# Kernel tuning notes

Hardware: AMD Instinct MI355X
Metric: run time of the kernel (lower is better)

The kernel has to match this reference:

```python
import jax, jax.numpy as jnp
import numpy as np

N = 100000      # nodes
E = 3200000     # edges (avg degree 32)
D = 128         # input feature dim
K = 8           # propagation hops
OUT = 128       # output size


def setup_inputs() -> dict:
    key = jax.random.key(0)
    k1, k2, k3, k4 = jax.random.split(key, 4)
    feature = jax.random.normal(k1, (N, D), dtype=jnp.float32)
    edge_index = jax.random.randint(k2, (2, E), 0, N, dtype=jnp.int32)
    # nn.Linear default init: U(-1/sqrt(fan_in), 1/sqrt(fan_in)), fan_in = D*(K+1)
    lim = 1.0 / np.sqrt(D * (K + 1))
    weight = jax.random.uniform(k3, (OUT, D * (K + 1)), minval=-lim, maxval=lim, dtype=jnp.float32)
    bias = jax.random.uniform(k4, (OUT,), minval=-lim, maxval=lim, dtype=jnp.float32)
    return {"feature": feature, "edge_index": edge_index, "weight": weight, "bias": bias}


def reference(feature, edge_index, weight, bias):
    # CombUnweighted: K hops of symmetric-normalized aggregation, concat all hops.
    row, col = edge_index[0], edge_index[1]  # source -> target
    n = feature.shape[0]
    deg = jax.ops.segment_sum(jnp.ones((row.shape[0],), dtype=feature.dtype), col, num_segments=n)
    dinv = jnp.where(deg > 0, jax.lax.rsqrt(jnp.maximum(deg, 1.0)), 0.0)
    norm = dinv[row] * dinv[col]  # [E]
    xs = [feature]
    x = feature
    for _ in range(K):
        msgs = x[row] * norm[:, None]                       # gather + scale: [E, D]
        x = jax.ops.segment_sum(msgs, col, num_segments=n)  # scatter-add:   [N, D]
        xs.append(x)
    h = jnp.concatenate(xs, axis=-1)  # [N, D*(K+1)]
    return h @ weight.T + bias        # [N, OUT]
```

## Files before the change

### kernel.cpp

```cpp
#include <hip/hip_runtime.h>

#define DFEAT 128
#define NHOPS 8
#define NOUT 128
#define DK (DFEAT*(NHOPS+1))

#define BN   512
#define CAPB 17408
#define PCH  4096

typedef __attribute__((ext_vector_type(8))) short short8;
typedef __attribute__((ext_vector_type(4))) float f32x4;
typedef __attribute__((ext_vector_type(2))) float f32x2;

static inline int cdiv(int a, int b){ return (a+b-1)/b; }

__device__ __forceinline__ unsigned short f2bf(float f){
  unsigned int u = __builtin_bit_cast(unsigned int, f);
  unsigned int lsb = (u >> 16) & 1u;
  u += 0x7fffu + lsb;
  return (unsigned short)(u >> 16);
}
__device__ __forceinline__ unsigned int pkbf16(float a, float b){
  unsigned int r;
  asm("v_cvt_pk_bf16_f32 %0, %1, %2" : "=v"(r) : "v"(a), "v"(b));
  return r;
}
__device__ __forceinline__ float cl448(float x){
  return fminf(fmaxf(x, -448.f), 448.f);
}

#if __has_builtin(__builtin_elementwise_fma)
#define PKFMA(a, f, w) (a) = __builtin_elementwise_fma((f), (w), (a))
#else
#define PKFMA(a, f, w) (a) = (f)*(w) + (a)
#endif

__device__ __forceinline__ int xcd_swz(int b, int nwg){
  int q = nwg >> 3, r = nwg & 7;
  int x = b & 7, o = b >> 3;
  return (x < r ? x*(q+1) : r*(q+1) + (x-r)*q) + o;
}


__global__ void k_binit(int* __restrict__ gcur, int nb){
  int b = blockIdx.x*256 + threadIdx.x;
  if(b < nb) gcur[b] = b*CAPB;
}

__global__ __launch_bounds__(256) void k_part(const int* __restrict__ row, const int* __restrict__ col,
                       int E, int nb, int* __restrict__ gcur, uint2* __restrict__ part){
  __shared__ int hist[256];
  __shared__ int lbase[256];
  __shared__ int gbase[256];
  __shared__ int cnt2[256];
  __shared__ uint2 stage[PCH];
  int t = threadIdx.x;
  int e0 = blockIdx.x*PCH;
  int ecnt = min(PCH, E - e0);
  hist[t] = 0; cnt2[t] = 0;
  __syncthreads();
  int es[PCH/256], et[PCH/256];
  #pragma unroll
  for(int i = 0; i < PCH/256; ++i){
    int li = t + i*256;
    if(li < ecnt){
      int e = e0 + li;
      es[i] = row[e]; et[i] = col[e];
      atomicAdd(&hist[et[i] >> 9], 1);
    } else et[i] = -1;
  }
  __syncthreads();
  int h = hist[t];
  lbase[t] = h; __syncthreads();
  #pragma unroll
  for(int off = 1; off < 256; off <<= 1){
    int y = (t >= off) ? lbase[t-off] : 0;
    __syncthreads();
    if(t >= off) lbase[t] += y;
    __syncthreads();
  }
  int incl = lbase[t];
  lbase[t] = incl - h;
  gbase[t] = (t < nb && h > 0) ? atomicAdd(&gcur[t], h) : 0;
  __syncthreads();
  #pragma unroll
  for(int i = 0; i < PCH/256; ++i){
    if(et[i] >= 0){
      int b = et[i] >> 9;
      int pos = lbase[b] + atomicAdd(&cnt2[b], 1);
      stage[pos] = (uint2){(unsigned)es[i], (unsigned)et[i]};
    }
  }
  __syncthreads();
  for(int i = t; i < ecnt; i += 256){
    uint2 p = stage[i];
    int b = (int)(p.y >> 9);
    part[(size_t)gbase[b] + (i - lbase[b])] = p;
  }
}

__global__ __launch_bounds__(256) void k_build(const uint2* __restrict__ part, const int* __restrict__ gcur,
                        int* __restrict__ offs, int* __restrict__ ends, float* __restrict__ dinv,
                        int* __restrict__ csr_row, int N){
  __shared__ int ncnt[BN];
  __shared__ int sc[BN];
  __shared__ int ncur[BN];
  __shared__ int psum[256];
  int b = blockIdx.x;
  int base = b*CAPB;
  int cnt = gcur[b] - base;
  int t = threadIdx.x;
  ncnt[t] = 0; ncnt[t+256] = 0;
  __syncthreads();
  for(int i = t; i < cnt; i += 256)
    atomicAdd(&ncnt[part[(size_t)base + i].y & (BN-1)], 1);
  __syncthreads();
  int a0 = ncnt[2*t], a1 = ncnt[2*t+1];
  psum[t] = a0 + a1; __syncthreads();
  #pragma unroll
  for(int off = 1; off < 256; off <<= 1){
    int y = (t >= off) ? psum[t-off] : 0;
    __syncthreads();
    if(t >= off) psum[t] += y;
    __syncthreads();
  }
  int ep = psum[t] - (a0 + a1);
  sc[2*t] = ep; sc[2*t+1] = ep + a0;
  __syncthreads();
  #pragma unroll
  for(int l = t; l < BN; l += 256){
    int node = b*BN + l;
    if(node < N){
      int c = ncnt[l];
      int o = base + sc[l];
      offs[node] = o; ends[node] = o + c;
      dinv[node] = c ? rsqrtf((float)c) : 0.f;
      ncur[l] = o;
    }
  }
  __syncthreads();
  for(int i = t; i < cnt; i += 256){
    uint2 p = part[(size_t)base + i];
    int pos = atomicAdd(&ncur[p.y & (BN-1)], 1);
    csr_row[pos] = (int)p.x;
  }
}


__global__ void k_castx(const float* __restrict__ src, unsigned char* __restrict__ f8,
                        int fstr, unsigned short* __restrict__ h0, int N){
  int tid = blockIdx.x*256 + threadIdx.x;
  if(tid >= N*8) return;
  int n = tid >> 3, sub = tid & 7;
  const float* s = src + (size_t)n*DFEAT + sub*16;
  float v[16];
  #pragma unroll
  for(int i = 0; i < 4; ++i){
    float4 x = *(const float4*)(s + i*4);
    v[i*4+0]=x.x; v[i*4+1]=x.y; v[i*4+2]=x.z; v[i*4+3]=x.w;
  }
  uint4 o8;
  o8.x = __builtin_amdgcn_cvt_pk_fp8_f32(cl448(v[0]),  cl448(v[1]),  0, false);
  o8.x = __builtin_amdgcn_cvt_pk_fp8_f32(cl448(v[2]),  cl448(v[3]),  o8.x, true);
  o8.y = __builtin_amdgcn_cvt_pk_fp8_f32(cl448(v[4]),  cl448(v[5]),  0, false);
  o8.y = __builtin_amdgcn_cvt_pk_fp8_f32(cl448(v[6]),  cl448(v[7]),  o8.y, true);
  o8.z = __builtin_amdgcn_cvt_pk_fp8_f32(cl448(v[8]),  cl448(v[9]),  0, false);
  o8.z = __builtin_amdgcn_cvt_pk_fp8_f32(cl448(v[10]), cl448(v[11]), o8.z, true);
  o8.w = __builtin_amdgcn_cvt_pk_fp8_f32(cl448(v[12]), cl448(v[13]), 0, false);
  o8.w = __builtin_amdgcn_cvt_pk_fp8_f32(cl448(v[14]), cl448(v[15]), o8.w, true);
  *(uint4*)(f8 + (size_t)n*fstr + sub*16) = o8;
  uint4 b0, b1;
  b0.x = pkbf16(v[0], v[1]);  b0.y = pkbf16(v[2], v[3]);
  b0.z = pkbf16(v[4], v[5]);  b0.w = pkbf16(v[6], v[7]);
  b1.x = pkbf16(v[8], v[9]);  b1.y = pkbf16(v[10],v[11]);
  b1.z = pkbf16(v[12],v[13]); b1.w = pkbf16(v[14],v[15]);
  uint4* hp = (uint4*)(h0 + (size_t)n*DFEAT + sub*16);
  hp[0] = b0; hp[1] = b1;
}

__global__ void k_castw(const float* __restrict__ src, unsigned short* __restrict__ dst, int n){
  int i4 = (blockIdx.x*256 + threadIdx.x) * 4;
  if(i4 >= n) return;
  int col = i4 % DK;
  float ex = fminf(2.5f * (float)(col >> 7), 7.0f);
  float sc = exp2f(-ex);
  float4 v = *(const float4*)(src + i4);
  unsigned short* d = dst + i4;
  d[0] = f2bf(v.x*sc); d[1] = f2bf(v.y*sc); d[2] = f2bf(v.z*sc); d[3] = f2bf(v.w*sc);
}


template<int FSTR>
__global__ __launch_bounds__(256) void k_hop(const unsigned char* __restrict__ fin,
                      unsigned char* __restrict__ fout,
                      unsigned short* __restrict__ hout,
                      const int* __restrict__ offs, const int* __restrict__ ends,
                      const int* __restrict__ csr_row, const float* __restrict__ dinv,
                      int N, float ratio){
  int bb = xcd_swz(blockIdx.x, gridDim.x);
  int wid  = (int)(((unsigned)bb*blockDim.x + threadIdx.x) >> 6);
  int lane = threadIdx.x & 63;
  if(wid >= N) return;
  int s = __builtin_amdgcn_readfirstlane(offs[wid]);
  int e = __builtin_amdgcn_readfirstlane(ends[wid]);
  float dt = __builtin_bit_cast(float, (int)__builtin_amdgcn_readfirstlane(__builtin_bit_cast(int, dinv[wid])));
  int g = lane >> 3, q = lane & 7;
  const unsigned char* xq = fin + q*16;
  f32x2 acc[8] = {};
  int full = s + ((e - s) & ~7);
  #pragma unroll 2
  for(int j = s; j < full; j += 8){
    int r = __builtin_nontemporal_load(csr_row + j + g);
    float w = dinv[r];
    uint4 v = *(const uint4*)(xq + (size_t)r*FSTR);
    f32x2 w2 = {w, w};
    f32x2 f;
    f = __builtin_amdgcn_cvt_pk_f32_fp8(v.x, false); PKFMA(acc[0], f, w2);
    f = __builtin_amdgcn_cvt_pk_f32_fp8(v.x, true);  PKFMA(acc[1], f, w2);
    f = __builtin_amdgcn_cvt_pk_f32_fp8(v.y, false); PKFMA(acc[2], f, w2);
    f = __builtin_amdgcn_cvt_pk_f32_fp8(v.y, true);  PKFMA(acc[3], f, w2);
    f = __builtin_amdgcn_cvt_pk_f32_fp8(v.z, false); PKFMA(acc[4], f, w2);
    f = __builtin_amdgcn_cvt_pk_f32_fp8(v.z, true);  PKFMA(acc[5], f, w2);
    f = __builtin_amdgcn_cvt_pk_f32_fp8(v.w, false); PKFMA(acc[6], f, w2);
    f = __builtin_amdgcn_cvt_pk_f32_fp8(v.w, true);  PKFMA(acc[7], f, w2);
  }
  if(full < e){
    int jj = full + g;
    bool live = jj < e;
    int r = live ? __builtin_nontemporal_load(csr_row + jj) : 0;
    float w = live ? dinv[r] : 0.f;
    uint4 v = *(const uint4*)(xq + (size_t)r*FSTR);
    f32x2 w2 = {w, w};
    f32x2 f;
    f = __builtin_amdgcn_cvt_pk_f32_fp8(v.x, false); PKFMA(acc[0], f, w2);
    f = __builtin_amdgcn_cvt_pk_f32_fp8(v.x, true);  PKFMA(acc[1], f, w2);
    f = __builtin_amdgcn_cvt_pk_f32_fp8(v.y, false); PKFMA(acc[2], f, w2);
    f = __builtin_amdgcn_cvt_pk_f32_fp8(v.y, true);  PKFMA(acc[3], f, w2);
    f = __builtin_amdgcn_cvt_pk_f32_fp8(v.z, false); PKFMA(acc[4], f, w2);
    f = __builtin_amdgcn_cvt_pk_f32_fp8(v.z, true);  PKFMA(acc[5], f, w2);
    f = __builtin_amdgcn_cvt_pk_f32_fp8(v.w, false); PKFMA(acc[6], f, w2);
    f = __builtin_amdgcn_cvt_pk_f32_fp8(v.w, true);  PKFMA(acc[7], f, w2);
  }
  float accs[16];
  #pragma unroll
  for(int i = 0; i < 8; ++i){ accs[2*i] = acc[i].x; accs[2*i+1] = acc[i].y; }
  #pragma unroll
  for(int d = 0; d < 16; ++d){
    accs[d] += __shfl_xor(accs[d], 8);
    accs[d] += __shfl_xor(accs[d], 16);
    accs[d] += __shfl_xor(accs[d], 32);
  }
  if(g == 0){
    float sA = dt * ratio;
    #pragma unroll
    for(int d = 0; d < 16; ++d) accs[d] = cl448(accs[d]*sA);
    uint4 o;
    o.x = __builtin_amdgcn_cvt_pk_fp8_f32(accs[0],  accs[1],  0, false);
    o.x = __builtin_amdgcn_cvt_pk_fp8_f32(accs[2],  accs[3],  o.x, true);
    o.y = __builtin_amdgcn_cvt_pk_fp8_f32(accs[4],  accs[5],  0, false);
    o.y = __builtin_amdgcn_cvt_pk_fp8_f32(accs[6],  accs[7],  o.y, true);
    o.z = __builtin_amdgcn_cvt_pk_fp8_f32(accs[8],  accs[9],  0, false);
    o.z = __builtin_amdgcn_cvt_pk_fp8_f32(accs[10], accs[11], o.z, true);
    o.w = __builtin_amdgcn_cvt_pk_fp8_f32(accs[12], accs[13], 0, false);
    o.w = __builtin_amdgcn_cvt_pk_fp8_f32(accs[14], accs[15], o.w, true);
    *(uint4*)(fout + (size_t)wid*FSTR + q*16) = o;
    if(hout){
      uint4 h0, h1;
      h0.x = pkbf16(accs[0],  accs[1]);  h0.y = pkbf16(accs[2],  accs[3]);
      h0.z = pkbf16(accs[4],  accs[5]);  h0.w = pkbf16(accs[6],  accs[7]);
      h1.x = pkbf16(accs[8],  accs[9]);  h1.y = pkbf16(accs[10], accs[11]);
      h1.z = pkbf16(accs[12], accs[13]); h1.w = pkbf16(accs[14], accs[15]);
      uint4* hp = (uint4*)(hout + (size_t)wid*DFEAT + q*16);
      hp[0] = h0; hp[1] = h1;
    }
  }
}


template<int ACC>
__global__ __launch_bounds__(256) void k_gemm(
    const unsigned short* __restrict__ Abf,
    const unsigned char*  __restrict__ Af8,
    int f8from, int k0W, int kcount,
    const unsigned short* __restrict__ Wb,
    const float* __restrict__ bias,
    float* __restrict__ out, int Nn)
{
  __shared__ unsigned short As[64*64];
  __shared__ unsigned short Bs[128*64];
  int t = threadIdx.x;
  int w = t >> 6, l = t & 63;
  int node0 = blockIdx.x * 64;
  int wm = (w >> 1) * 32;
  int wn = (w & 1) * 64;
  int lr = l & 15, lg = l >> 4;

  f32x4 acc[2][4] = {};

  for(int kc0 = 0; kc0 < kcount; kc0 += 64){
    if(kc0 >= f8from){
      #pragma unroll
      for(int it = 0; it < 2; ++it){
        int flat = it*256 + t;
        int row = flat >> 3, kk = (flat & 7) << 3;
        int nn = node0 + row;
        uint2 v = {0u, 0u};
        if(nn < Nn) v = *(const uint2*)(Af8 + (size_t)nn*DK + kc0 + kk);
        f32x2 f0 = __builtin_amdgcn_cvt_pk_f32_fp8(v.x, false);
        f32x2 f1 = __builtin_amdgcn_cvt_pk_f32_fp8(v.x, true);
        f32x2 f2 = __builtin_amdgcn_cvt_pk_f32_fp8(v.y, false);
        f32x2 f3 = __builtin_amdgcn_cvt_pk_f32_fp8(v.y, true);
        uint4 bv;
        bv.x = pkbf16(f0.x, f0.y); bv.y = pkbf16(f1.x, f1.y);
        bv.z = pkbf16(f2.x, f2.y); bv.w = pkbf16(f3.x, f3.y);
        unsigned int bo = ((unsigned int)row << 7) + ((unsigned int)kk << 1);
        bo ^= (unsigned int)(row & 7) << 4;
        *(uint4*)((char*)As + bo) = bv;
      }
    } else {
      #pragma unroll
      for(int it = 0; it < 2; ++it){
        int flat = it*256 + t;
        int row = flat >> 3, kk = (flat & 7) << 3;
        float4 v = {0.f,0.f,0.f,0.f};
        int nn = node0 + row;
        if(nn < Nn) v = *(const float4*)(Abf + (size_t)nn*DFEAT + kc0 + kk);
        unsigned int bo = ((unsigned int)row << 7) + ((unsigned int)kk << 1);
        bo ^= (unsigned int)(row & 7) << 4;
        *(float4*)((char*)As + bo) = v;
      }
    }
    #pragma unroll
    for(int it = 0; it < 4; ++it){
      int flat = it*256 + t;
      int row = flat >> 3, kk = (flat & 7) << 3;
      float4 v = *(const float4*)(Wb + (size_t)row*DK + k0W + kc0 + kk);
      unsigned int bo = ((unsigned int)row << 7) + ((unsigned int)kk << 1);
      bo ^= (unsigned int)(row & 7) << 4;
      *(float4*)((char*)Bs + bo) = v;
    }
    __syncthreads();
    #pragma unroll
    for(int ks = 0; ks < 2; ++ks){
      short8 af[2], bfr[4];
      #pragma unroll
      for(int mi = 0; mi < 2; ++mi){
        int row = wm + mi*16 + lr;
        unsigned int bo = ((unsigned int)row << 7) + (unsigned int)(ks*64 + lg*16);
        bo ^= (unsigned int)(row & 7) << 4;
        af[mi] = *(const short8*)((const char*)As + bo);
      }
      #pragma unroll
      for(int ni = 0; ni < 4; ++ni){
        int row = wn + ni*16 + lr;
        unsigned int bo = ((unsigned int)row << 7) + (unsigned int)(ks*64 + lg*16);
        bo ^= (unsigned int)(row & 7) << 4;
        bfr[ni] = *(const short8*)((const char*)Bs + bo);
      }
      #pragma unroll
      for(int mi = 0; mi < 2; ++mi)
        #pragma unroll
        for(int ni = 0; ni < 4; ++ni)
          acc[mi][ni] = __builtin_amdgcn_mfma_f32_16x16x32_bf16(af[mi], bfr[ni], acc[mi][ni], 0, 0, 0);
    }
    __syncthreads();
  }

  int r0 = lg << 2;
  #pragma unroll
  for(int mi = 0; mi < 2; ++mi){
    #pragma unroll
    for(int ni = 0; ni < 4; ++ni){
      int col = wn + ni*16 + lr;
      #pragma unroll
      for(int r = 0; r < 4; ++r){
        int rr = node0 + wm + mi*16 + r0 + r;
        if(rr < Nn){
          float* po = out + (size_t)rr*NOUT + col;
          float v = acc[mi][ni][r];
          if(ACC) *po += v;
          else    *po = v + bias[col];
        }
      }
    }
  }
}


extern "C" void kernel_launch(void* const* d_in, const int* in_sizes, int n_in,
                              void* d_out, int out_size, void* d_ws, size_t ws_size,
                              hipStream_t stream){
  const float* feat = (const float*)d_in[0];
  const int*   ei   = (const int*)d_in[1];
  const float* W    = (const float*)d_in[2];
  const float* bias = (const float*)d_in[3];
  float* out = (float*)d_out;

  int N = in_sizes[0] / DFEAT;
  int E = in_sizes[1] / 2;
  const int* rowv = ei;
  const int* colv = ei + E;
  int nb = cdiv(N, BN);

  char* p = (char*)d_ws;
  size_t used = 0;
  auto carve = [&](size_t bytes)->char*{
    char* q = p; size_t b = (bytes + 255) & ~size_t(255); p += b; used += b; return q;
  };
  int*   gcur    = (int*)  carve((size_t)nb*4);
  int*   offs    = (int*)  carve((size_t)N*4);
  int*   ends    = (int*)  carve((size_t)N*4);
  float* dinv    = (float*)carve((size_t)N*4);
  int*   csr_row = (int*)  carve((size_t)nb*CAPB*4);
  unsigned short* Wb = (unsigned short*)carve((size_t)NOUT*DK*2);
  unsigned short* H0 = (unsigned short*)carve((size_t)N*DFEAT*2);

  size_t partBytes = (size_t)nb*CAPB*8;
  size_t f8aBytes  = (size_t)N*DK;
  size_t f8sBytes  = (size_t)N*DFEAT;
  size_t bsBytes   = (size_t)N*DFEAT*2;

  size_t unionBytes = f8aBytes > partBytes ? f8aBytes : partBytes;
  bool pathA = (used + unionBytes) <= ws_size;

  uint2* part;
  unsigned char* F8 = nullptr;
  unsigned char *fA = nullptr, *fB = nullptr;
  unsigned short *bb0 = nullptr, *bb1 = nullptr;
  if(pathA){
    char* un = carve(unionBytes);
    part = (uint2*)un;
    F8   = (unsigned char*)un;
  } else {
    part = (uint2*)carve(partBytes);
    fA  = (unsigned char*)carve(f8sBytes);
    fB  = (unsigned char*)carve(f8sBytes);
    bb0 = (unsigned short*)carve(bsBytes);
    bb1 = (unsigned short*)carve(bsBytes);
  }

  k_binit<<<cdiv(nb,256), 256, 0, stream>>>(gcur, nb);
  k_part <<<cdiv(E,PCH), 256, 0, stream>>>(rowv, colv, E, nb, gcur, part);
  k_build<<<nb, 256, 0, stream>>>(part, gcur, offs, ends, dinv, csr_row, N);

  k_castw<<<cdiv(NOUT*DK/4,256), 256, 0, stream>>>(W, Wb, NOUT*DK);

  int gemm_grid = cdiv(N, 64);
  int hop_grid  = cdiv(N, 4);
  int cast_grid = cdiv(N*8, 256);

  float sprev = 1.0f;
  float ratios[NHOPS+1];
  for(int k = 1; k <= NHOPS; ++k){
    float ex = 2.5f*(float)k; if(ex > 7.0f) ex = 7.0f;
    float sk = exp2f(ex);
    ratios[k] = sk / sprev;
    sprev = sk;
  }

  if(pathA){
    k_castx<<<cast_grid, 256, 0, stream>>>(feat, F8, DK, H0, N);
    for(int k = 1; k <= NHOPS; ++k){
      k_hop<DK><<<hop_grid, 256, 0, stream>>>(F8 + (size_t)(k-1)*DFEAT, F8 + (size_t)k*DFEAT,
                                              nullptr, offs, ends, csr_row, dinv, N, ratios[k]);
    }
    k_gemm<0><<<gemm_grid, 256, 0, stream>>>(H0, F8, DFEAT, 0, DK, Wb, bias, out, N);
  } else {
    k_castx<<<cast_grid, 256, 0, stream>>>(feat, fA, DFEAT, H0, N);
    k_gemm<0><<<gemm_grid, 256, 0, stream>>>(H0, nullptr, 1<<30, 0, DFEAT, Wb, bias, out, N);
    unsigned char* cur = fA;
    for(int k = 1; k <= NHOPS; ++k){
      unsigned char* nxt = (k & 1) ? fB : fA;
      unsigned short* hs = (k & 1) ? bb1 : bb0;
      k_hop<DFEAT><<<hop_grid, 256, 0, stream>>>(cur, nxt, hs, offs, ends, csr_row, dinv, N, ratios[k]);
      k_gemm<1><<<gemm_grid, 256, 0, stream>>>(hs, nullptr, 1<<30, k*DFEAT, DFEAT, Wb, bias, out, N);
      cur = nxt;
    }
  }
}
```

Baseline: 710.2 us.

## Store degree-prescaled hop features to drop per-edge dinv gather

Each hop's features are now stored pre-multiplied by the source node's inverse sqrt degree (x·dinv). The gather loop therefore sums raw fp8 rows without loading dinv[r] for every edge, and the node scale becomes dinv². The GEMM undoes the prescale by multiplying the fp8 operand by sqrt(degree), and weights for hops ≥1 carry an extra 0.25 factor to offset the 4x fp8 prescale. This removes a random per-edge 4-byte load and the FMA weight, at the cost of a shifted fp8 dynamic range and an extra per-row scale in the GEMM A-load.

```diff
diff --git a/kernel.cpp b/kernel.cpp
--- a/kernel.cpp
+++ b/kernel.cpp
@@ -102,7 +102,7 @@
 
 __global__ __launch_bounds__(256) void k_build(const uint2* __restrict__ part, const int* __restrict__ gcur,
                         int* __restrict__ offs, int* __restrict__ ends, float* __restrict__ dinv,
-                        int* __restrict__ csr_row, int N){
+                        float* __restrict__ sdeg, int* __restrict__ csr_row, int N){
   __shared__ int ncnt[BN];
   __shared__ int sc[BN];
   __shared__ int ncur[BN];
@@ -136,6 +136,7 @@
       int o = base + sc[l];
       offs[node] = o; ends[node] = o + c;
       dinv[node] = c ? rsqrtf((float)c) : 0.f;
+      sdeg[node] = c ? sqrtf((float)c) : 0.f;
       ncur[l] = o;
     }
   }
@@ -148,12 +149,14 @@
 }
 
 
-__global__ void k_castx(const float* __restrict__ src, unsigned char* __restrict__ f8,
+__global__ void k_castx(const float* __restrict__ src, const float* __restrict__ dinv,
+                        unsigned char* __restrict__ f8,
                         int fstr, unsigned short* __restrict__ h0, int N){
   int tid = blockIdx.x*256 + threadIdx.x;
   if(tid >= N*8) return;
   int n = tid >> 3, sub = tid & 7;
   const float* s = src + (size_t)n*DFEAT + sub*16;
+  float sc0 = dinv[n] * 4.0f;
   float v[16];
   #pragma unroll
   for(int i = 0; i < 4; ++i){
@@ -161,14 +164,14 @@
     v[i*4+0]=x.x; v[i*4+1]=x.y; v[i*4+2]=x.z; v[i*4+3]=x.w;
   }
   uint4 o8;
-  o8.x = __builtin_amdgcn_cvt_pk_fp8_f32(cl448(v[0]),  cl448(v[1]),  0, false);
-  o8.x = __builtin_amdgcn_cvt_pk_fp8_f32(cl448(v[2]),  cl448(v[3]),  o8.x, true);
-  o8.y = __builtin_amdgcn_cvt_pk_fp8_f32(cl448(v[4]),  cl448(v[5]),  0, false);
-  o8.y = __builtin_amdgcn_cvt_pk_fp8_f32(cl448(v[6]),  cl448(v[7]),  o8.y, true);
-  o8.z = __builtin_amdgcn_cvt_pk_fp8_f32(cl448(v[8]),  cl448(v[9]),  0, false);
-  o8.z = __builtin_amdgcn_cvt_pk_fp8_f32(cl448(v[10]), cl448(v[11]), o8.z, true);
-  o8.w = __builtin_amdgcn_cvt_pk_fp8_f32(cl448(v[12]), cl448(v[13]), 0, false);
-  o8.w = __builtin_amdgcn_cvt_pk_fp8_f32(cl448(v[14]), cl448(v[15]), o8.w, true);
+  o8.x = __builtin_amdgcn_cvt_pk_fp8_f32(cl448(v[0]*sc0),  cl448(v[1]*sc0),  0, false);
+  o8.x = __builtin_amdgcn_cvt_pk_fp8_f32(cl448(v[2]*sc0),  cl448(v[3]*sc0),  o8.x, true);
+  o8.y = __builtin_amdgcn_cvt_pk_fp8_f32(cl448(v[4]*sc0),  cl448(v[5]*sc0),  0, false);
+  o8.y = __builtin_amdgcn_cvt_pk_fp8_f32(cl448(v[6]*sc0),  cl448(v[7]*sc0),  o8.y, true);
+  o8.z = __builtin_amdgcn_cvt_pk_fp8_f32(cl448(v[8]*sc0),  cl448(v[9]*sc0),  0, false);
+  o8.z = __builtin_amdgcn_cvt_pk_fp8_f32(cl448(v[10]*sc0), cl448(v[11]*sc0), o8.z, true);
+  o8.w = __builtin_amdgcn_cvt_pk_fp8_f32(cl448(v[12]*sc0), cl448(v[13]*sc0), 0, false);
+  o8.w = __builtin_amdgcn_cvt_pk_fp8_f32(cl448(v[14]*sc0), cl448(v[15]*sc0), o8.w, true);
   *(uint4*)(f8 + (size_t)n*fstr + sub*16) = o8;
   uint4 b0, b1;
   b0.x = pkbf16(v[0], v[1]);  b0.y = pkbf16(v[2], v[3]);
@@ -183,8 +186,10 @@
   int i4 = (blockIdx.x*256 + threadIdx.x) * 4;
   if(i4 >= n) return;
   int col = i4 % DK;
-  float ex = fminf(2.5f * (float)(col >> 7), 7.0f);
+  int k = col >> 7;
+  float ex = fminf(2.5f * (float)k, 7.0f);
   float sc = exp2f(-ex);
+  if(k) sc *= 0.25f;
   float4 v = *(const float4*)(src + i4);
   unsigned short* d = dst + i4;
   d[0] = f2bf(v.x*sc); d[1] = f2bf(v.y*sc); d[2] = f2bf(v.z*sc); d[3] = f2bf(v.w*sc);
@@ -212,7 +217,22 @@
   #pragma unroll 2
   for(int j = s; j < full; j += 8){
     int r = __builtin_nontemporal_load(csr_row + j + g);
-    float w = dinv[r];
+    uint4 v = *(const uint4*)(xq + (size_t)r*FSTR);
+    f32x2 f;
+    f = __builtin_amdgcn_cvt_pk_f32_fp8(v.x, false); acc[0] += f;
+    f = __builtin_amdgcn_cvt_pk_f32_fp8(v.x, true);  acc[1] += f;
+    f = __builtin_amdgcn_cvt_pk_f32_fp8(v.y, false); acc[2] += f;
+    f = __builtin_amdgcn_cvt_pk_f32_fp8(v.y, true);  acc[3] += f;
+    f = __builtin_amdgcn_cvt_pk_f32_fp8(v.z, false); acc[4] += f;
+    f = __builtin_amdgcn_cvt_pk_f32_fp8(v.z, true);  acc[5] += f;
+    f = __builtin_amdgcn_cvt_pk_f32_fp8(v.w, false); acc[6] += f;
+    f = __builtin_amdgcn_cvt_pk_f32_fp8(v.w, true);  acc[7] += f;
+  }
+  if(full < e){
+    int jj = full + g;
+    bool live = jj < e;
+    int r = live ? __builtin_nontemporal_load(csr_row + jj) : 0;
+    float w = live ? 1.f : 0.f;
     uint4 v = *(const uint4*)(xq + (size_t)r*FSTR);
     f32x2 w2 = {w, w};
     f32x2 f;
@@ -225,23 +245,6 @@
     f = __builtin_amdgcn_cvt_pk_f32_fp8(v.w, false); PKFMA(acc[6], f, w2);
     f = __builtin_amdgcn_cvt_pk_f32_fp8(v.w, true);  PKFMA(acc[7], f, w2);
   }
-  if(full < e){
-    int jj = full + g;
-    bool live = jj < e;
-    int r = live ? __builtin_nontemporal_load(csr_row + jj) : 0;
-    float w = live ? dinv[r] : 0.f;
-    uint4 v = *(const uint4*)(xq + (size_t)r*FSTR);
-    f32x2 w2 = {w, w};
-    f32x2 f;
-    f = __builtin_amdgcn_cvt_pk_f32_fp8(v.x, false); PKFMA(acc[0], f, w2);
-    f = __builtin_amdgcn_cvt_pk_f32_fp8(v.x, true);  PKFMA(acc[1], f, w2);
-    f = __builtin_amdgcn_cvt_pk_f32_fp8(v.y, false); PKFMA(acc[2], f, w2);
-    f = __builtin_amdgcn_cvt_pk_f32_fp8(v.y, true);  PKFMA(acc[3], f, w2);
-    f = __builtin_amdgcn_cvt_pk_f32_fp8(v.z, false); PKFMA(acc[4], f, w2);
-    f = __builtin_amdgcn_cvt_pk_f32_fp8(v.z, true);  PKFMA(acc[5], f, w2);
-    f = __builtin_amdgcn_cvt_pk_f32_fp8(v.w, false); PKFMA(acc[6], f, w2);
-    f = __builtin_amdgcn_cvt_pk_f32_fp8(v.w, true);  PKFMA(acc[7], f, w2);
-  }
   float accs[16];
   #pragma unroll
   for(int i = 0; i < 8; ++i){ accs[2*i] = acc[i].x; accs[2*i+1] = acc[i].y; }
@@ -252,25 +255,27 @@
     accs[d] += __shfl_xor(accs[d], 32);
   }
   if(g == 0){
-    float sA = dt * ratio;
+    float sA = dt * dt * ratio;
+    float a8[16];
     #pragma unroll
-    for(int d = 0; d < 16; ++d) accs[d] = cl448(accs[d]*sA);
+    for(int d = 0; d < 16; ++d) a8[d] = cl448(accs[d]*sA);
     uint4 o;
-    o.x = __builtin_amdgcn_cvt_pk_fp8_f32(accs[0],  accs[1],  0, false);
-    o.x = __builtin_amdgcn_cvt_pk_fp8_f32(accs[2],  accs[3],  o.x, true);
-    o.y = __builtin_amdgcn_cvt_pk_fp8_f32(accs[4],  accs[5],  0, false);
-    o.y = __builtin_amdgcn_cvt_pk_fp8_f32(accs[6],  accs[7],  o.y, true);
-    o.z = __builtin_amdgcn_cvt_pk_fp8_f32(accs[8],  accs[9],  0, false);
-    o.z = __builtin_amdgcn_cvt_pk_fp8_f32(accs[10], accs[11], o.z, true);
-    o.w = __builtin_amdgcn_cvt_pk_fp8_f32(accs[12], accs[13], 0, false);
-    o.w = __builtin_amdgcn_cvt_pk_fp8_f32(accs[14], accs[15], o.w, true);
+    o.x = __builtin_amdgcn_cvt_pk_fp8_f32(a8[0],  a8[1],  0, false);
+    o.x = __builtin_amdgcn_cvt_pk_fp8_f32(a8[2],  a8[3],  o.x, true);
+    o.y = __builtin_amdgcn_cvt_pk_fp8_f32(a8[4],  a8[5],  0, false);
+    o.y = __builtin_amdgcn_cvt_pk_fp8_f32(a8[6],  a8[7],  o.y, true);
+    o.z = __builtin_amdgcn_cvt_pk_fp8_f32(a8[8],  a8[9],  0, false);
+    o.z = __builtin_amdgcn_cvt_pk_fp8_f32(a8[10], a8[11], o.z, true);
+    o.w = __builtin_amdgcn_cvt_pk_fp8_f32(a8[12], a8[13], 0, false);
+    o.w = __builtin_amdgcn_cvt_pk_fp8_f32(a8[14], a8[15], o.w, true);
     *(uint4*)(fout + (size_t)wid*FSTR + q*16) = o;
     if(hout){
+      float sB = dt * ratio;
       uint4 h0, h1;
-      h0.x = pkbf16(accs[0],  accs[1]);  h0.y = pkbf16(accs[2],  accs[3]);
-      h0.z = pkbf16(accs[4],  accs[5]);  h0.w = pkbf16(accs[6],  accs[7]);
-      h1.x = pkbf16(accs[8],  accs[9]);  h1.y = pkbf16(accs[10], accs[11]);
-      h1.z = pkbf16(accs[12], accs[13]); h1.w = pkbf16(accs[14], accs[15]);
+      h0.x = pkbf16(accs[0]*sB,  accs[1]*sB);  h0.y = pkbf16(accs[2]*sB,  accs[3]*sB);
+      h0.z = pkbf16(accs[4]*sB,  accs[5]*sB);  h0.w = pkbf16(accs[6]*sB,  accs[7]*sB);
+      h1.x = pkbf16(accs[8]*sB,  accs[9]*sB);  h1.y = pkbf16(accs[10]*sB, accs[11]*sB);
+      h1.z = pkbf16(accs[12]*sB, accs[13]*sB); h1.w = pkbf16(accs[14]*sB, accs[15]*sB);
       uint4* hp = (uint4*)(hout + (size_t)wid*DFEAT + q*16);
       hp[0] = h0; hp[1] = h1;
     }
@@ -282,6 +287,7 @@
 __global__ __launch_bounds__(256) void k_gemm(
     const unsigned short* __restrict__ Abf,
     const unsigned char*  __restrict__ Af8,
+    const float* __restrict__ rs,
     int f8from, int k0W, int kcount,
     const unsigned short* __restrict__ Wb,
     const float* __restrict__ bias,
@@ -306,14 +312,15 @@
         int row = flat >> 3, kk = (flat & 7) << 3;
         int nn = node0 + row;
         uint2 v = {0u, 0u};
-        if(nn < Nn) v = *(const uint2*)(Af8 + (size_t)nn*DK + kc0 + kk);
+        float rsv = 0.f;
+        if(nn < Nn){ v = *(const uint2*)(Af8 + (size_t)nn*DK + kc0 + kk); rsv = rs[nn]; }
         f32x2 f0 = __builtin_amdgcn_cvt_pk_f32_fp8(v.x, false);
         f32x2 f1 = __builtin_amdgcn_cvt_pk_f32_fp8(v.x, true);
         f32x2 f2 = __builtin_amdgcn_cvt_pk_f32_fp8(v.y, false);
         f32x2 f3 = __builtin_amdgcn_cvt_pk_f32_fp8(v.y, true);
         uint4 bv;
-        bv.x = pkbf16(f0.x, f0.y); bv.y = pkbf16(f1.x, f1.y);
-        bv.z = pkbf16(f2.x, f2.y); bv.w = pkbf16(f3.x, f3.y);
+        bv.x = pkbf16(f0.x*rsv, f0.y*rsv); bv.y = pkbf16(f1.x*rsv, f1.y*rsv);
+        bv.z = pkbf16(f2.x*rsv, f2.y*rsv); bv.w = pkbf16(f3.x*rsv, f3.y*rsv);
         unsigned int bo = ((unsigned int)row << 7) + ((unsigned int)kk << 1);
         bo ^= (unsigned int)(row & 7) << 4;
         *(uint4*)((char*)As + bo) = bv;
@@ -412,6 +419,7 @@
   int*   offs    = (int*)  carve((size_t)N*4);
   int*   ends    = (int*)  carve((size_t)N*4);
   float* dinv    = (float*)carve((size_t)N*4);
+  float* sdeg    = (float*)carve((size_t)N*4);
   int*   csr_row = (int*)  carve((size_t)nb*CAPB*4);
   unsigned short* Wb = (unsigned short*)carve((size_t)NOUT*DK*2);
   unsigned short* H0 = (unsigned short*)carve((size_t)N*DFEAT*2);
@@ -442,7 +450,7 @@
 
   k_binit<<<cdiv(nb,256), 256, 0, stream>>>(gcur, nb);
   k_part <<<cdiv(E,PCH), 256, 0, stream>>>(rowv, colv, E, nb, gcur, part);
-  k_build<<<nb, 256, 0, stream>>>(part, gcur, offs, ends, dinv, csr_row, N);
+  k_build<<<nb, 256, 0, stream>>>(part, gcur, offs, ends, dinv, sdeg, csr_row, N);
 
   k_castw<<<cdiv(NOUT*DK/4,256), 256, 0, stream>>>(W, Wb, NOUT*DK);
 
@@ -460,21 +468,21 @@
   }
 
   if(pathA){
-    k_castx<<<cast_grid, 256, 0, stream>>>(feat, F8, DK, H0, N);
+    k_castx<<<cast_grid, 256, 0, stream>>>(feat, dinv, F8, DK, H0, N);
     for(int k = 1; k <= NHOPS; ++k){
       k_hop<DK><<<hop_grid, 256, 0, stream>>>(F8 + (size_t)(k-1)*DFEAT, F8 + (size_t)k*DFEAT,
                                               nullptr, offs, ends, csr_row, dinv, N, ratios[k]);
     }
-    k_gemm<0><<<gemm_grid, 256, 0, stream>>>(H0, F8, DFEAT, 0, DK, Wb, bias, out, N);
+    k_gemm<0><<<gemm_grid, 256, 0, stream>>>(H0, F8, sdeg, DFEAT, 0, DK, Wb, bias, out, N);
   } else {
-    k_castx<<<cast_grid, 256, 0, stream>>>(feat, fA, DFEAT, H0, N);
-    k_gemm<0><<<gemm_grid, 256, 0, stream>>>(H0, nullptr, 1<<30, 0, DFEAT, Wb, bias, out, N);
+    k_castx<<<cast_grid, 256, 0, stream>>>(feat, dinv, fA, DFEAT, H0, N);
+    k_gemm<0><<<gemm_grid, 256, 0, stream>>>(H0, nullptr, sdeg, 1<<30, 0, DFEAT, Wb, bias, out, N);
     unsigned char* cur = fA;
     for(int k = 1; k <= NHOPS; ++k){
       unsigned char* nxt = (k & 1) ? fB : fA;
       unsigned short* hs = (k & 1) ? bb1 : bb0;
       k_hop<DFEAT><<<hop_grid, 256, 0, stream>>>(cur, nxt, hs, offs, ends, csr_row, dinv, N, ratios[k]);
-      k_gemm<1><<<gemm_grid, 256, 0, stream>>>(hs, nullptr, 1<<30, k*DFEAT, DFEAT, Wb, bias, out, N);
+      k_gemm<1><<<gemm_grid, 256, 0, stream>>>(hs, nullptr, sdeg, 1<<30, k*DFEAT, DFEAT, Wb, bias, out, N);
       cur = nxt;
     }
   }
```

Result: faster. 687.7 us (-3.2%).
